# Kernel tuning notes

Measured on AMD Instinct MI355X. Metric: run time of the kernel, lower is better.

Reference implementation:

```python
import jax, jax.numpy as jnp
from jax import lax
import numpy as np

PROPRIO = 48
NPTS = 1024
NP_PROX = 512
NP_DIST = 512
HP = 187  # proximal_feature_dim
HD = 64   # distal_feature_dim
B = 2048
NA = 12
ACTOR_DIMS = [PROPRIO + HP + HD, 1024, 512, 256, 128, NA]


def gru_last(x, wih, whh, bih, bhh):
    """torch-style GRU (gate order r,z,n), returns last hidden. x: [B,T,in]."""
    Bx, T, _ = x.shape
    H = whh.shape[1]
    gx = x @ wih.T + bih  # [B,T,3H], input projections precomputed
    def step(h, gxt):
        gh = h @ whh.T + bhh
        r = jax.nn.sigmoid(gxt[:, :H] + gh[:, :H])
        z = jax.nn.sigmoid(gxt[:, H:2 * H] + gh[:, H:2 * H])
        n = jnp.tanh(gxt[:, 2 * H:] + r * gh[:, 2 * H:])
        return (1.0 - z) * n + z * h, None
    h0 = jnp.zeros((Bx, H), x.dtype)
    hT, _ = lax.scan(step, h0, jnp.swapaxes(gx, 0, 1))
    return hT


def _encode(pts, w1, b1, w2, b2):
    h = jax.nn.elu(pts @ w1.T + b1)
    return jax.nn.elu(h @ w2.T + b2)


def _forward(obs, pe_prox_w1, pe_prox_b1, pe_prox_w2, pe_prox_b2,
             pe_dist_w1, pe_dist_b1, pe_dist_w2, pe_dist_b2,
             gru_prox_wih, gru_prox_whh, gru_prox_bih, gru_prox_bhh,
             gru_dist_wih, gru_dist_whh, gru_dist_bih, gru_dist_bhh,
             mem_prox_wih, mem_prox_whh, mem_prox_bih, mem_prox_bhh,
             mem_dist_wih, mem_dist_whh, mem_dist_bih, mem_dist_bhh,
             actor_w0, actor_b0, actor_w1, actor_b1, actor_w2, actor_b2,
             actor_w3, actor_b3, actor_w4, actor_b4,
             prox_idx, dist_idx):
    proprio = obs[:, :PROPRIO]
    lidar = obs[:, PROPRIO:].reshape(obs.shape[0], NPTS, 3)  # history_length=1
    # irregular gather of proximal/distal point subsets (sampling plan buffers)
    prox_enc = _encode(lidar[:, prox_idx], pe_prox_w1, pe_prox_b1, pe_prox_w2, pe_prox_b2)  # [B,512,64]
    dist_enc = _encode(lidar[:, dist_idx], pe_dist_w1, pe_dist_b1, pe_dist_w2, pe_dist_b2)  # [B,512,64]
    # spatial GRUs over the point sequence
    hp = gru_last(prox_enc, gru_prox_wih, gru_prox_whh, gru_prox_bih, gru_prox_bhh)  # [B,187]
    hd = gru_last(dist_enc, gru_dist_wih, gru_dist_whh, gru_dist_bih, gru_dist_bhh)  # [B,64]
    # temporal memory GRUs (single step, zero initial hidden)
    fp = gru_last(hp[:, None, :], mem_prox_wih, mem_prox_whh, mem_prox_bih, mem_prox_bhh)
    fd = gru_last(hd[:, None, :], mem_dist_wih, mem_dist_whh, mem_dist_bih, mem_dist_bhh)
    x = jnp.concatenate([proprio, fp, fd], axis=-1)  # [B,299]
    for w, b in ((actor_w0, actor_b0), (actor_w1, actor_b1), (actor_w2, actor_b2), (actor_w3, actor_b3)):
        x = jax.nn.elu(x @ w.T + b)
    return x @ actor_w4.T + actor_b4  # action mean [B,12]


def setup_inputs() -> dict:
    key = jax.random.key(0)
    ks = iter(jax.random.split(key, 64))
    def n(shape, scale=0.05):
        return (jax.random.normal(next(ks), shape, jnp.float32) * scale)
    inp = {}
    inp["obs"] = jax.random.normal(next(ks), (B, PROPRIO + NPTS * 3), jnp.float32)
    inp["prox_idx"] = jax.random.randint(next(ks), (NP_PROX,), 0, NPTS)
    inp["dist_idx"] = jax.random.randint(next(ks), (NP_DIST,), 0, NPTS)
    for pfx in ("pe_prox", "pe_dist"):
        inp[pfx + "_w1"] = n((64, 3)); inp[pfx + "_b1"] = jnp.zeros((64,), jnp.float32)
        inp[pfx + "_w2"] = n((64, 64)); inp[pfx + "_b2"] = jnp.zeros((64,), jnp.float32)
    for pfx, H, din in (("gru_prox", HP, 64), ("gru_dist", HD, 64), ("mem_prox", HP, HP), ("mem_dist", HD, HD)):
        inp[pfx + "_wih"] = n((3 * H, din)); inp[pfx + "_whh"] = n((3 * H, H))
        inp[pfx + "_bih"] = jnp.zeros((3 * H,), jnp.float32); inp[pfx + "_bhh"] = jnp.zeros((3 * H,), jnp.float32)
    for i, (di, do) in enumerate(zip(ACTOR_DIMS[:-1], ACTOR_DIMS[1:])):
        inp[f"actor_w{i}"] = n((do, di)); inp[f"actor_b{i}"] = jnp.zeros((do,), jnp.float32)
    return inp


def reference(obs, prox_idx, dist_idx,
              pe_prox_w1, pe_prox_b1, pe_prox_w2, pe_prox_b2,
              pe_dist_w1, pe_dist_b1, pe_dist_w2, pe_dist_b2,
              gru_prox_wih, gru_prox_whh, gru_prox_bih, gru_prox_bhh,
              gru_dist_wih, gru_dist_whh, gru_dist_bih, gru_dist_bhh,
              mem_prox_wih, mem_prox_whh, mem_prox_bih, mem_prox_bhh,
              mem_dist_wih, mem_dist_whh, mem_dist_bih, mem_dist_bhh,
              actor_w0, actor_b0, actor_w1, actor_b1, actor_w2, actor_b2,
              actor_w3, actor_b3, actor_w4, actor_b4):
    return _forward(obs, pe_prox_w1, pe_prox_b1, pe_prox_w2, pe_prox_b2,
                    pe_dist_w1, pe_dist_b1, pe_dist_w2, pe_dist_b2,
                    gru_prox_wih, gru_prox_whh, gru_prox_bih, gru_prox_bhh,
                    gru_dist_wih, gru_dist_whh, gru_dist_bih, gru_dist_bhh,
                    mem_prox_wih, mem_prox_whh, mem_prox_bih, mem_prox_bhh,
                    mem_dist_wih, mem_dist_whh, mem_dist_bih, mem_dist_bhh,
                    actor_w0, actor_b0, actor_w1, actor_b1, actor_w2, actor_b2,
                    actor_w3, actor_b3, actor_w4, actor_b4,
                    prox_idx, dist_idx)
```

## Files before the change

### kernel.cpp

```cpp
#include <hip/hip_runtime.h>
#include <stdint.h>

typedef __attribute__((ext_vector_type(8))) short short8;
typedef __attribute__((ext_vector_type(4))) float f32x4;

#define DEV __device__ __forceinline__

#define L2E 1.4426950408889634f

DEV unsigned short f2bf(float f) {
    union { float f; uint32_t u; } v; v.f = f;
    return (unsigned short)((v.u + 0x7FFFu + ((v.u >> 16) & 1u)) >> 16);
}
DEV float sig_(float x) {
    return __builtin_amdgcn_rcpf(1.f + __builtin_amdgcn_exp2f(-L2E * x));
}
DEV float tanh_(float x) {
    return 1.f - 2.f * __builtin_amdgcn_rcpf(1.f + __builtin_amdgcn_exp2f(2.f * L2E * x));
}
DEV float elu_(float x) {
    return x > 0.f ? x : __builtin_amdgcn_exp2f(L2E * x) - 1.f;
}
DEV f32x4 splat4(float v) { f32x4 r; r[0]=v; r[1]=v; r[2]=v; r[3]=v; return r; }
DEV void pin(short8& v) { asm volatile("" : "+v"(v)); }

struct PJob { const float* s; unsigned short* d; int Hs, NG, Ks, Kd, total; };
struct PJobs { PJob j[11]; };

__global__ __launch_bounds__(256) void pack_all(PJobs P)
{
    PJob jb = P.j[blockIdx.y];
    int e = blockIdx.x * 256 + threadIdx.x;
    if (e >= jb.total) return;
    int n = e / jb.Kd, k = e - n * jb.Kd;
    int g = n / jb.NG, jj = n - g * jb.NG;
    float v = (jj < jb.Hs && k < jb.Ks) ? jb.s[(size_t)(g * jb.Hs + jj) * jb.Ks + k] : 0.f;
    jb.d[e] = f2bf(v);
}

template<int H, int KP>
DEV void gru_body(int blk,
                  const float* __restrict__ obs, const int* __restrict__ idx,
                  const float* __restrict__ w1, const float* __restrict__ b1,
                  const float* __restrict__ w2, const float* __restrict__ b2,
                  const unsigned short* __restrict__ wih, const unsigned short* __restrict__ whh,
                  const float* __restrict__ bih, const float* __restrict__ bhh,
                  unsigned short* __restrict__ houtb, char* smem)
{
    constexpr int NCT = KP / 16;
    constexpr int KS  = KP / 32;
    constexpr int HP8 = KP + 8;

    unsigned short* hlds = (unsigned short*)(smem);
    unsigned short* xs   = (unsigned short*)(smem + 12800);
    unsigned short* h1s  = (unsigned short*)(smem + 17408);
    unsigned short* w2s  = (unsigned short*)(smem + 22016);
    float* ptsb          = (float*)(smem + 31232);
    float* w1s           = (float*)(smem + 31744);
    float* b1s           = (float*)(smem + 32768);
    float* b2s           = (float*)(smem + 33024);

    const int tid  = threadIdx.x;
    const int wave = tid >> 6, lane = tid & 63, quad = lane >> 4, l16 = lane & 15;
    const int b0   = blk * 16;
    const int ct   = wave;
    const bool act = (ct < NCT);
    const int c    = ct * 16 + l16;

    for (int e = tid; e < 2*16*HP8; e += 768) hlds[e] = 0;
    for (int e = tid; e < 4096; e += 768) { int n = e >> 6, k = e & 63; w2s[n*72 + k] = f2bf(w2[e]); }
    if (tid < 192) w1s[(tid/3)*4 + (tid - (tid/3)*3)] = w1[tid];
    if (tid < 64) { b1s[tid] = b1[tid]; b2s[tid] = b2[tid]; }

    const float* myrow = obs + (size_t)(b0 + (tid & 15)) * 3120 + 48;
    float px = 0.f, py = 0.f, pz = 0.f;
    if (tid < 16) {
        int p0 = idx[0];
        ptsb[tid*4 + 0] = myrow[3*p0 + 0];
        ptsb[tid*4 + 1] = myrow[3*p0 + 1];
        ptsb[tid*4 + 2] = myrow[3*p0 + 2];
        int p1 = idx[1];
        px = myrow[3*p1 + 0]; py = myrow[3*p1 + 1]; pz = myrow[3*p1 + 2];
    }

    short8 whr[3][KS];
    short8 wxr[3][2];
    float bsr = 0.f, bsz = 0.f, binx = 0.f, bhnn = 0.f;
    {
        const int cl = act ? c : l16;
#pragma unroll
        for (int g = 0; g < 3; ++g) {
#pragma unroll
            for (int ks = 0; ks < KS; ++ks)
                whr[g][ks] = *(const short8*)(whh + ((size_t)(g*KP + cl))*KP + ks*32 + quad*8);
#pragma unroll
            for (int ks = 0; ks < 2; ++ks)
                wxr[g][ks] = *(const short8*)(wih + ((size_t)(g*KP + cl))*64 + ks*32 + quad*8);
        }
    }
#pragma unroll
    for (int g = 0; g < 3; ++g) {
#pragma unroll
        for (int ks = 0; ks < KS; ++ks) pin(whr[g][ks]);
#pragma unroll
        for (int ks = 0; ks < 2; ++ks)  pin(wxr[g][ks]);
    }
    if (act && c < H) {
        bsr  = bih[c]       + bhh[c];
        bsz  = bih[H + c]   + bhh[H + c];
        binx = bih[2*H + c];
        bhnn = bhh[2*H + c];
    }
    float hreg[4] = {0.f, 0.f, 0.f, 0.f};

    __syncthreads();

    int cur = 0;
    for (int i = 0; i < 514; ++i) {
        if (i < 512) {
            const float* pt = ptsb + (i & 1) * 64;
            unsigned short* h1w = h1s + (i & 1) * (16*72);
#pragma unroll
            for (int e = tid; e < 1024; e += 768) {
                int p = e >> 6, ch = e & 63;
                float v = w1s[ch*4+0]*pt[p*4+0] + w1s[ch*4+1]*pt[p*4+1]
                        + w1s[ch*4+2]*pt[p*4+2] + b1s[ch];
                h1w[p*72 + ch] = f2bf(elu_(v));
            }
            if (tid < 16) {
                float* dst = ptsb + ((i+1) & 1) * 64 + tid*4;
                dst[0] = px; dst[1] = py; dst[2] = pz;
                int tn = (i + 2 < 512) ? i + 2 : 511;
                int pn = idx[tn];
                px = myrow[3*pn + 0]; py = myrow[3*pn + 1]; pz = myrow[3*pn + 2];
            }
        }
        if (i >= 1 && i < 513 && wave < 4) {
            const unsigned short* h1r = h1s + ((i-1) & 1) * (16*72);
            unsigned short*       xw  = xs  + ((i-1) & 1) * (16*72);
            f32x4 a2 = splat4(0.f);
#pragma unroll
            for (int ks = 0; ks < 2; ++ks) {
                short8 af = *(const short8*)(h1r + l16*72 + ks*32 + quad*8);
                short8 bf = *(const short8*)(w2s + (wave*16 + l16)*72 + ks*32 + quad*8);
                a2 = __builtin_amdgcn_mfma_f32_16x16x32_bf16(af, bf, a2, 0, 0, 0);
            }
            int c2 = wave*16 + l16;
            float b2v = b2s[c2];
#pragma unroll
            for (int j = 0; j < 4; ++j)
                xw[(quad*4 + j)*72 + c2] = f2bf(elu_(a2[j] + b2v));
        }
        if (i >= 2) {
            int t = i - 2;
            const unsigned short* xsr = xs + (t & 1) * (16*72);
            const unsigned short* hc  = hlds + cur * (16*HP8);
            unsigned short*       hn  = hlds + (cur ^ 1) * (16*HP8);
            if (act) {
                f32x4 acc[4];
                acc[0] = splat4(bsr);
                acc[1] = splat4(bsz);
                acc[2] = splat4(binx);
                acc[3] = splat4(bhnn);
#pragma unroll
                for (int ks = 0; ks < 2; ++ks) {
                    short8 xf = *(const short8*)(xsr + l16*72 + ks*32 + quad*8);
                    acc[0] = __builtin_amdgcn_mfma_f32_16x16x32_bf16(xf, wxr[0][ks], acc[0], 0, 0, 0);
                    acc[1] = __builtin_amdgcn_mfma_f32_16x16x32_bf16(xf, wxr[1][ks], acc[1], 0, 0, 0);
                    acc[2] = __builtin_amdgcn_mfma_f32_16x16x32_bf16(xf, wxr[2][ks], acc[2], 0, 0, 0);
                }
#pragma unroll
                for (int ks = 0; ks < KS; ++ks) {
                    short8 ah = *(const short8*)(hc + l16*HP8 + ks*32 + quad*8);
                    acc[0] = __builtin_amdgcn_mfma_f32_16x16x32_bf16(ah, whr[0][ks], acc[0], 0, 0, 0);
                    acc[1] = __builtin_amdgcn_mfma_f32_16x16x32_bf16(ah, whr[1][ks], acc[1], 0, 0, 0);
                    acc[3] = __builtin_amdgcn_mfma_f32_16x16x32_bf16(ah, whr[2][ks], acc[3], 0, 0, 0);
                }
#pragma unroll
                for (int j = 0; j < 4; ++j) {
                    int m = quad*4 + j;
                    float r  = sig_(acc[0][j]);
                    float zg = sig_(acc[1][j]);
                    float nn = tanh_(acc[2][j] + r * acc[3][j]);
                    float hv = nn + zg * (hreg[j] - nn);
                    hreg[j] = hv;
                    hn[m*HP8 + c] = f2bf(hv);
                }
            }
            cur ^= 1;
        }
        __syncthreads();
    }

    if (act)
#pragma unroll
        for (int j = 0; j < 4; ++j) {
            int m = quad*4 + j;
            houtb[(size_t)(b0 + m)*KP + c] = (c < H) ? f2bf(hreg[j]) : 0;
        }
}

__global__ __launch_bounds__(768)
__attribute__((amdgpu_waves_per_eu(3, 3)))
void gru_kernel(
    const float* __restrict__ obs,
    const int* __restrict__ prox_idx, const int* __restrict__ dist_idx,
    const float* __restrict__ w1p, const float* __restrict__ b1p,
    const float* __restrict__ w2p, const float* __restrict__ b2p,
    const float* __restrict__ w1d, const float* __restrict__ b1d,
    const float* __restrict__ w2d, const float* __restrict__ b2d,
    const unsigned short* __restrict__ wihp, const unsigned short* __restrict__ whhp,
    const unsigned short* __restrict__ wihd, const unsigned short* __restrict__ whhd,
    const float* __restrict__ bihp, const float* __restrict__ bhhp,
    const float* __restrict__ bihd, const float* __restrict__ bhhd,
    unsigned short* __restrict__ hpb, unsigned short* __restrict__ hdb)
{
    __shared__ __align__(16) char smem[33280];
    if (blockIdx.x < 128)
        gru_body<187, 192>(blockIdx.x, obs, prox_idx, w1p, b1p, w2p, b2p,
                           wihp, whhp, bihp, bhhp, hpb, smem);
    else
        gru_body<64, 64>(blockIdx.x - 128, obs, dist_idx, w1d, b1d, w2d, b2d,
                         wihd, whhd, bihd, bhhd, hdb, smem);
}

__global__ __launch_bounds__(256) void bgemm_kernel(
    const unsigned short* __restrict__ A, const unsigned short* __restrict__ B,
    const float* __restrict__ bias, void* __restrict__ C,
    int Kp, int Np, int Nstore, int mode)
{
    __shared__ __align__(16) unsigned short Asl[64*40];
    __shared__ __align__(16) unsigned short Bsl[64*40];
    const int tid = threadIdx.x;
    const int wave = tid >> 6, lane = tid & 63, quad = lane >> 4, l16 = lane & 15;
    const int n0 = blockIdx.x * 64, m0 = blockIdx.y * 64;
    const int r = tid >> 2, sg = (tid & 3) * 8;

    f32x4 acc[4];
#pragma unroll
    for (int nt = 0; nt < 4; ++nt) acc[nt] = splat4(0.f);

    for (int k0 = 0; k0 < Kp; k0 += 32) {
        short8 av = *(const short8*)(A + (size_t)(m0 + r)*Kp + k0 + sg);
        short8 bv;
        if (n0 + r < Np) bv = *(const short8*)(B + (size_t)(n0 + r)*Kp + k0 + sg);
        else { short8 z; for (int q = 0; q < 8; ++q) z[q] = 0; bv = z; }
        *(short8*)(Asl + r*40 + sg) = av;
        *(short8*)(Bsl + r*40 + sg) = bv;
        __syncthreads();
        short8 af = *(const short8*)(Asl + (wave*16 + l16)*40 + quad*8);
#pragma unroll
        for (int nt = 0; nt < 4; ++nt) {
            short8 bf = *(const short8*)(Bsl + (nt*16 + l16)*40 + quad*8);
            acc[nt] = __builtin_amdgcn_mfma_f32_16x16x32_bf16(af, bf, acc[nt], 0, 0, 0);
        }
        __syncthreads();
    }
#pragma unroll
    for (int nt = 0; nt < 4; ++nt) {
        int n = n0 + nt*16 + l16;
        float bv = (bias && n < Np) ? bias[n] : 0.f;
#pragma unroll
        for (int j = 0; j < 4; ++j) {
            int m = m0 + wave*16 + quad*4 + j;
            float v = acc[nt][j] + bv;
            if (mode == 1) {
                ((unsigned short*)C)[(size_t)m*Np + n] = f2bf(elu_(v));
            } else {
                if (n < Nstore) ((float*)C)[(size_t)m*Nstore + n] = v;
            }
        }
    }
}

__global__ __launch_bounds__(256) void memcat_kernel(
    const float* __restrict__ obs, const float* __restrict__ Gp, const float* __restrict__ Gd,
    const float* __restrict__ mbip, const float* __restrict__ mbhp,
    const float* __restrict__ mbid, const float* __restrict__ mbhd,
    unsigned short* __restrict__ x0b)
{
    int i = blockIdx.x * 256 + threadIdx.x;
    if (i >= 2048 * 320) return;
    int b = i / 320, cc = i - b * 320;
    float v;
    if (cc < 48) {
        v = obs[(size_t)b*3120 + cc];
    } else if (cc < 235) {
        int j = cc - 48;
        float dr = Gp[(size_t)b*576 + j];
        float dz = Gp[(size_t)b*576 + 192 + j];
        float dn = Gp[(size_t)b*576 + 384 + j];
        float r  = sig_(dr + mbip[j] + mbhp[j]);
        float zg = sig_(dz + mbip[187+j] + mbhp[187+j]);
        float nn = tanh_(dn + mbip[374+j] + r * mbhp[374+j]);
        v = (1.f - zg) * nn;
    } else if (cc < 299) {
        int j = cc - 235;
        float dr = Gd[(size_t)b*192 + j];
        float dz = Gd[(size_t)b*192 + 64 + j];
        float dn = Gd[(size_t)b*192 + 128 + j];
        float r  = sig_(dr + mbid[j] + mbhd[j]);
        float zg = sig_(dz + mbid[64+j] + mbhd[64+j]);
        float nn = tanh_(dn + mbid[128+j] + r * mbhd[128+j]);
        v = (1.f - zg) * nn;
    } else {
        v = 0.f;
    }
    x0b[i] = f2bf(v);
}

extern "C" void kernel_launch(void* const* d_in, const int* in_sizes, int n_in,
                              void* d_out, int out_size, void* d_ws, size_t ws_size,
                              hipStream_t stream)
{
    (void)in_sizes; (void)n_in; (void)out_size; (void)ws_size;
    const float* obs        = (const float*)d_in[0];
    const int*   prox_idx   = (const int*)d_in[1];
    const int*   dist_idx   = (const int*)d_in[2];
    const float* pe_prox_w1 = (const float*)d_in[3];
    const float* pe_prox_b1 = (const float*)d_in[4];
    const float* pe_prox_w2 = (const float*)d_in[5];
    const float* pe_prox_b2 = (const float*)d_in[6];
    const float* pe_dist_w1 = (const float*)d_in[7];
    const float* pe_dist_b1 = (const float*)d_in[8];
    const float* pe_dist_w2 = (const float*)d_in[9];
    const float* pe_dist_b2 = (const float*)d_in[10];
    const float* gp_wih = (const float*)d_in[11];
    const float* gp_whh = (const float*)d_in[12];
    const float* gp_bih = (const float*)d_in[13];
    const float* gp_bhh = (const float*)d_in[14];
    const float* gd_wih = (const float*)d_in[15];
    const float* gd_whh = (const float*)d_in[16];
    const float* gd_bih = (const float*)d_in[17];
    const float* gd_bhh = (const float*)d_in[18];
    const float* mp_wih = (const float*)d_in[19];
    const float* mp_bih = (const float*)d_in[21];
    const float* mp_bhh = (const float*)d_in[22];
    const float* md_wih = (const float*)d_in[23];
    const float* md_bih = (const float*)d_in[25];
    const float* md_bhh = (const float*)d_in[26];
    const float* aw0 = (const float*)d_in[27]; const float* ab0 = (const float*)d_in[28];
    const float* aw1 = (const float*)d_in[29]; const float* ab1 = (const float*)d_in[30];
    const float* aw2 = (const float*)d_in[31]; const float* ab2 = (const float*)d_in[32];
    const float* aw3 = (const float*)d_in[33]; const float* ab3 = (const float*)d_in[34];
    const float* aw4 = (const float*)d_in[35]; const float* ab4 = (const float*)d_in[36];
    float* out = (float*)d_out;

    char* ws = (char*)d_ws;
    size_t off = 0;
    auto alloc = [&](size_t bytes) -> char* {
        char* p = ws + off;
        off = (off + bytes + 255) & ~(size_t)255;
        return p;
    };
    unsigned short* wih_p = (unsigned short*)alloc(36864*2);
    unsigned short* whh_p = (unsigned short*)alloc(110592*2);
    unsigned short* wih_d = (unsigned short*)alloc(12288*2);
    unsigned short* whh_d = (unsigned short*)alloc(12288*2);
    unsigned short* mw_p  = (unsigned short*)alloc(110592*2);
    unsigned short* mw_d  = (unsigned short*)alloc(12288*2);
    unsigned short* w0p   = (unsigned short*)alloc((size_t)1024*320*2);
    unsigned short* w1p   = (unsigned short*)alloc((size_t)512*1024*2);
    unsigned short* w2p   = (unsigned short*)alloc((size_t)256*512*2);
    unsigned short* w3p   = (unsigned short*)alloc((size_t)128*256*2);
    unsigned short* w4p   = (unsigned short*)alloc((size_t)16*128*2);
    unsigned short* hpb   = (unsigned short*)alloc((size_t)2048*192*2);
    unsigned short* hdb   = (unsigned short*)alloc((size_t)2048*64*2);
    float* Gp             = (float*)alloc((size_t)2048*576*4);
    float* Gd             = (float*)alloc((size_t)2048*192*4);
    unsigned short* x0b   = (unsigned short*)alloc((size_t)2048*320*2);
    unsigned short* a1b   = (unsigned short*)alloc((size_t)2048*1024*2);
    unsigned short* a2b   = (unsigned short*)alloc((size_t)2048*512*2);
    unsigned short* a3b   = (unsigned short*)alloc((size_t)2048*256*2);
    unsigned short* a4b   = (unsigned short*)alloc((size_t)2048*128*2);

    PJobs P;
    P.j[0]  = { gp_wih, wih_p, 187, 192, 64, 64, 36864 };
    P.j[1]  = { gp_whh, whh_p, 187, 192, 187, 192, 110592 };
    P.j[2]  = { gd_wih, wih_d, 64, 64, 64, 64, 12288 };
    P.j[3]  = { gd_whh, whh_d, 64, 64, 64, 64, 12288 };
    P.j[4]  = { mp_wih, mw_p, 187, 192, 187, 192, 110592 };
    P.j[5]  = { md_wih, mw_d, 64, 64, 64, 64, 12288 };
    P.j[6]  = { aw0, w0p, 1024, 1024, 299, 320, 327680 };
    P.j[7]  = { aw1, w1p, 512, 512, 1024, 1024, 524288 };
    P.j[8]  = { aw2, w2p, 256, 256, 512, 512, 131072 };
    P.j[9]  = { aw3, w3p, 128, 128, 256, 256, 32768 };
    P.j[10] = { aw4, w4p, 12, 16, 128, 128, 2048 };
    pack_all<<<dim3(2048, 11), 256, 0, stream>>>(P);

    gru_kernel<<<256, 768, 0, stream>>>(
        obs, prox_idx, dist_idx,
        pe_prox_w1, pe_prox_b1, pe_prox_w2, pe_prox_b2,
        pe_dist_w1, pe_dist_b1, pe_dist_w2, pe_dist_b2,
        wih_p, whh_p, wih_d, whh_d,
        gp_bih, gp_bhh, gd_bih, gd_bhh, hpb, hdb);

    bgemm_kernel<<<dim3(9, 32), 256, 0, stream>>>(hpb, mw_p, nullptr, Gp, 192, 576, 576, 0);
    bgemm_kernel<<<dim3(3, 32), 256, 0, stream>>>(hdb, mw_d, nullptr, Gd, 64, 192, 192, 0);
    memcat_kernel<<<2560, 256, 0, stream>>>(obs, Gp, Gd, mp_bih, mp_bhh, md_bih, md_bhh, x0b);

    bgemm_kernel<<<dim3(16, 32), 256, 0, stream>>>(x0b, w0p, ab0, a1b, 320, 1024, 1024, 1);
    bgemm_kernel<<<dim3(8,  32), 256, 0, stream>>>(a1b, w1p, ab1, a2b, 1024, 512, 512, 1);
    bgemm_kernel<<<dim3(4,  32), 256, 0, stream>>>(a2b, w2p, ab2, a3b, 512, 256, 256, 1);
    bgemm_kernel<<<dim3(2,  32), 256, 0, stream>>>(a3b, w3p, ab3, a4b, 256, 128, 128, 1);
    bgemm_kernel<<<dim3(1,  32), 256, 0, stream>>>(a4b, w4p, ab4, out, 128, 16, 12, 0);
}
```

Before: 867.8 us.

## Precompute proximal point encodings in FP8 and run GRU input projection with FP8 MFMA

Adds a separate encoder kernel that gathers proximal lidar points, runs the two-layer ELU point MLP, and stores the encodings as FP8 in workspace. The proximal GRU then streams these FP8 encodings, keeps the FP8-packed input weights in registers, and uses FP8 MFMA for the input projection, taking the per-step encoder work off the serial recurrence. It also drops the waves_per_eu attribute. The costs are an extra 64MB write and read of encodings, an extra launch, reduced precision on the GRU inputs and weights, and a fallback to the fused path if the workspace is too small.

```diff
diff --git a/kernel.cpp b/kernel.cpp
--- a/kernel.cpp
+++ b/kernel.cpp
@@ -3,6 +3,7 @@
 
 typedef __attribute__((ext_vector_type(8))) short short8;
 typedef __attribute__((ext_vector_type(4))) float f32x4;
+typedef __attribute__((ext_vector_type(4))) unsigned int u32x4;
 
 #define DEV __device__ __forceinline__
 
@@ -12,6 +13,26 @@
     union { float f; uint32_t u; } v; v.f = f;
     return (unsigned short)((v.u + 0x7FFFu + ((v.u >> 16) & 1u)) >> 16);
 }
+DEV uint8_t f2fp8(float f) {
+    union { float f; uint32_t u; } v; v.f = f;
+    uint32_t s = (v.u >> 24) & 0x80u;
+    uint32_t absu = v.u & 0x7FFFFFFFu;
+    int E = (int)(absu >> 23);
+    if (E >= 135 + 1) return (uint8_t)(s | 0x7E);
+    if (E >= 121) {
+        uint32_t m = absu & 0x7FFFFFu;
+        uint32_t keep = m >> 20;
+        uint32_t rest = m & 0xFFFFFu;
+        uint32_t rnd = (rest > 0x80000u || (rest == 0x80000u && (keep & 1u))) ? 1u : 0u;
+        uint32_t mag = (((uint32_t)(E - 120) << 3) | keep) + rnd;
+        if (mag > 0x7Eu) mag = 0x7Eu;
+        return (uint8_t)(s | mag);
+    }
+    float sc = __builtin_fabsf(f) * 512.f;
+    uint32_t m8 = (uint32_t)(sc + 0.5f);
+    if (m8 > 7u) return (uint8_t)(s | 0x08);
+    return (uint8_t)(s | m8);
+}
 DEV float sig_(float x) {
     return __builtin_amdgcn_rcpf(1.f + __builtin_amdgcn_exp2f(-L2E * x));
 }
@@ -23,9 +44,10 @@
 }
 DEV f32x4 splat4(float v) { f32x4 r; r[0]=v; r[1]=v; r[2]=v; r[3]=v; return r; }
 DEV void pin(short8& v) { asm volatile("" : "+v"(v)); }
+DEV void pinl(long& v)  { asm volatile("" : "+v"(v)); }
 
 struct PJob { const float* s; unsigned short* d; int Hs, NG, Ks, Kd, total; };
-struct PJobs { PJob j[11]; };
+struct PJobs { PJob j[12]; };
 
 __global__ __launch_bounds__(256) void pack_all(PJobs P)
 {
@@ -38,8 +60,172 @@
     jb.d[e] = f2bf(v);
 }
 
+__global__ __launch_bounds__(256) void pack_fp8(const float* __restrict__ src,
+                                                uint8_t* __restrict__ dst)
+{
+    int e = blockIdx.x * 256 + threadIdx.x;
+    if (e >= 576 * 64) return;
+    int n = e >> 6, k = e & 63;
+    int g = n / 192, jj = n - g * 192;
+    float v = (jj < 187) ? src[(size_t)(g * 187 + jj) * 64 + k] : 0.f;
+    dst[e] = f2fp8(v);
+}
+
+__global__ __launch_bounds__(256) void enc_kernel(
+    const float* __restrict__ obs, const int* __restrict__ idx,
+    const float* __restrict__ w1, const float* __restrict__ b1,
+    const unsigned short* __restrict__ w2p, const float* __restrict__ b2,
+    uint8_t* __restrict__ enc8)
+{
+    const int b = blockIdx.x, t0 = blockIdx.y * 64;
+    const int tid = threadIdx.x;
+    __shared__ __align__(16) float pts[64][4];
+    __shared__ float w1s[256];
+    __shared__ float b1s[64], b2s[64];
+    __shared__ __align__(16) unsigned short h1s[64][72];
+
+    if (tid < 192) w1s[(tid/3)*4 + (tid - (tid/3)*3)] = w1[tid];
+    if (tid < 64) { b1s[tid] = b1[tid]; b2s[tid] = b2[tid]; }
+    for (int e = tid; e < 192; e += 256) {
+        int p = e / 3, c2 = e - p * 3;
+        int pi = idx[t0 + p];
+        pts[p][c2] = obs[(size_t)b * 3120 + 48 + (size_t)pi * 3 + c2];
+    }
+    __syncthreads();
+#pragma unroll
+    for (int r = 0; r < 16; ++r) {
+        int e = tid + r * 256;
+        int p = e >> 6, ch = e & 63;
+        float v = w1s[ch*4]*pts[p][0] + w1s[ch*4+1]*pts[p][1]
+                + w1s[ch*4+2]*pts[p][2] + b1s[ch];
+        h1s[p][ch] = f2bf(elu_(v));
+    }
+    __syncthreads();
+    const int wave = tid >> 6, lane = tid & 63, quad = lane >> 4, l16 = lane & 15;
+#pragma unroll
+    for (int ct = 0; ct < 4; ++ct) {
+        f32x4 a2 = splat4(0.f);
+#pragma unroll
+        for (int ks = 0; ks < 2; ++ks) {
+            short8 af = *(const short8*)(&h1s[wave*16 + l16][ks*32 + quad*8]);
+            short8 bf = *(const short8*)(w2p + (ct*16 + l16)*64 + ks*32 + quad*8);
+            a2 = __builtin_amdgcn_mfma_f32_16x16x32_bf16(af, bf, a2, 0, 0, 0);
+        }
+        int c = ct*16 + l16;
+        float b2v = b2s[c];
+#pragma unroll
+        for (int j = 0; j < 4; ++j) {
+            int m = wave*16 + quad*4 + j;
+            enc8[((size_t)b*512 + t0 + m)*64 + c] = f2fp8(elu_(a2[j] + b2v));
+        }
+    }
+}
+
+DEV void gru_body_pre(int blk, const uint8_t* __restrict__ enc8,
+                      const uint8_t* __restrict__ wih8,
+                      const unsigned short* __restrict__ whh,
+                      const float* __restrict__ bih, const float* __restrict__ bhh,
+                      unsigned short* __restrict__ houtb, char* smem)
+{
+    constexpr int H = 187, KP = 192, KS = 6, HP8 = 200;
+    unsigned short* hlds = (unsigned short*)smem;
+    uint8_t* xs = (uint8_t*)(smem + 12800);
+
+    const int tid  = threadIdx.x;
+    const int wave = tid >> 6, lane = tid & 63, quad = lane >> 4, l16 = lane & 15;
+    const int b0   = blk * 16;
+    const int c    = wave * 16 + l16;
+
+    for (int e = tid; e < 2*16*HP8; e += 768) hlds[e] = 0;
+
+    short8 whr[3][KS];
+    long   wx8[3][2];
+#pragma unroll
+    for (int g = 0; g < 3; ++g) {
+#pragma unroll
+        for (int ks = 0; ks < KS; ++ks)
+            whr[g][ks] = *(const short8*)(whh + ((size_t)(g*KP + c))*KP + ks*32 + quad*8);
+#pragma unroll
+        for (int ks = 0; ks < 2; ++ks)
+            wx8[g][ks] = *(const long*)(wih8 + ((size_t)(g*KP + c))*64 + ks*32 + quad*8);
+    }
+#pragma unroll
+    for (int g = 0; g < 3; ++g) {
+#pragma unroll
+        for (int ks = 0; ks < KS; ++ks) pin(whr[g][ks]);
+#pragma unroll
+        for (int ks = 0; ks < 2; ++ks)  pinl(wx8[g][ks]);
+    }
+    float bsr = 0.f, bsz = 0.f, binx = 0.f, bhnn = 0.f;
+    if (c < H) {
+        bsr  = bih[c]       + bhh[c];
+        bsz  = bih[H + c]   + bhh[H + c];
+        binx = bih[2*H + c];
+        bhnn = bhh[2*H + c];
+    }
+    float hreg[4] = {0.f, 0.f, 0.f, 0.f};
+
+    u32x4 xq;
+    const int xrow = lane >> 2, xseg = lane & 3;
+    if (wave == 0) {
+        xq = *(const u32x4*)(enc8 + ((size_t)(b0 + xrow)*512 + 0)*64 + xseg*16);
+        *(u32x4*)(xs + 0*1280 + xrow*80 + xseg*16) = xq;
+        xq = *(const u32x4*)(enc8 + ((size_t)(b0 + xrow)*512 + 1)*64 + xseg*16);
+    }
+    __syncthreads();
+
+    int cur = 0;
+    for (int t = 0; t < 512; ++t) {
+        if (wave == 0) {
+            *(u32x4*)(xs + ((t+1)&1)*1280 + xrow*80 + xseg*16) = xq;
+            int tn = (t + 2 < 512) ? t + 2 : 511;
+            xq = *(const u32x4*)(enc8 + ((size_t)(b0 + xrow)*512 + tn)*64 + xseg*16);
+        }
+        const uint8_t* xsr = xs + (t&1)*1280;
+        const unsigned short* hc = hlds + cur * (16*HP8);
+        unsigned short*       hn = hlds + (cur ^ 1) * (16*HP8);
+
+        f32x4 acc[4];
+        acc[0] = splat4(bsr);
+        acc[1] = splat4(bsz);
+        acc[2] = splat4(binx);
+        acc[3] = splat4(bhnn);
+#pragma unroll
+        for (int ks = 0; ks < 2; ++ks) {
+            long a8 = *(const long*)(xsr + l16*80 + ks*32 + quad*8);
+            acc[0] = __builtin_amdgcn_mfma_f32_16x16x32_fp8_fp8(a8, wx8[0][ks], acc[0], 0, 0, 0);
+            acc[1] = __builtin_amdgcn_mfma_f32_16x16x32_fp8_fp8(a8, wx8[1][ks], acc[1], 0, 0, 0);
+            acc[2] = __builtin_amdgcn_mfma_f32_16x16x32_fp8_fp8(a8, wx8[2][ks], acc[2], 0, 0, 0);
+        }
+#pragma unroll
+        for (int ks = 0; ks < KS; ++ks) {
+            short8 ah = *(const short8*)(hc + l16*HP8 + ks*32 + quad*8);
+            acc[0] = __builtin_amdgcn_mfma_f32_16x16x32_bf16(ah, whr[0][ks], acc[0], 0, 0, 0);
+            acc[1] = __builtin_amdgcn_mfma_f32_16x16x32_bf16(ah, whr[1][ks], acc[1], 0, 0, 0);
+            acc[3] = __builtin_amdgcn_mfma_f32_16x16x32_bf16(ah, whr[2][ks], acc[3], 0, 0, 0);
+        }
+#pragma unroll
+        for (int j = 0; j < 4; ++j) {
+            int m = quad*4 + j;
+            float r  = sig_(acc[0][j]);
+            float zg = sig_(acc[1][j]);
+            float nn = tanh_(acc[2][j] + r * acc[3][j]);
+            float hv = nn + zg * (hreg[j] - nn);
+            hreg[j] = hv;
+            hn[m*HP8 + c] = f2bf(hv);
+        }
+        cur ^= 1;
+        __syncthreads();
+    }
+#pragma unroll
+    for (int j = 0; j < 4; ++j) {
+        int m = quad*4 + j;
+        houtb[(size_t)(b0 + m)*KP + c] = (c < H) ? f2bf(hreg[j]) : 0;
+    }
+}
+
 template<int H, int KP>
-DEV void gru_body(int blk,
+DEV void gru_body_fused(int blk,
                   const float* __restrict__ obs, const int* __restrict__ idx,
                   const float* __restrict__ w1, const float* __restrict__ b1,
                   const float* __restrict__ w2, const float* __restrict__ b2,
@@ -200,11 +386,11 @@
         }
 }
 
-__global__ __launch_bounds__(768)
-__attribute__((amdgpu_waves_per_eu(3, 3)))
-void gru_kernel(
+__global__ __launch_bounds__(768) void gru_kernel(
+    int mode,
     const float* __restrict__ obs,
     const int* __restrict__ prox_idx, const int* __restrict__ dist_idx,
+    const uint8_t* __restrict__ encp8, const uint8_t* __restrict__ wihp8,
     const float* __restrict__ w1p, const float* __restrict__ b1p,
     const float* __restrict__ w2p, const float* __restrict__ b2p,
     const float* __restrict__ w1d, const float* __restrict__ b1d,
@@ -216,12 +402,16 @@
     unsigned short* __restrict__ hpb, unsigned short* __restrict__ hdb)
 {
     __shared__ __align__(16) char smem[33280];
-    if (blockIdx.x < 128)
-        gru_body<187, 192>(blockIdx.x, obs, prox_idx, w1p, b1p, w2p, b2p,
-                           wihp, whhp, bihp, bhhp, hpb, smem);
-    else
-        gru_body<64, 64>(blockIdx.x - 128, obs, dist_idx, w1d, b1d, w2d, b2d,
-                         wihd, whhd, bihd, bhhd, hdb, smem);
+    if (blockIdx.x < 128) {
+        if (mode == 0)
+            gru_body_pre(blockIdx.x, encp8, wihp8, whhp, bihp, bhhp, hpb, smem);
+        else
+            gru_body_fused<187, 192>(blockIdx.x, obs, prox_idx, w1p, b1p, w2p, b2p,
+                                     wihp, whhp, bihp, bhhp, hpb, smem);
+    } else {
+        gru_body_fused<64, 64>(blockIdx.x - 128, obs, dist_idx, w1d, b1d, w2d, b2d,
+                               wihd, whhd, bihd, bhhd, hdb, smem);
+    }
 }
 
 __global__ __launch_bounds__(256) void bgemm_kernel(
@@ -313,7 +503,7 @@
                               void* d_out, int out_size, void* d_ws, size_t ws_size,
                               hipStream_t stream)
 {
-    (void)in_sizes; (void)n_in; (void)out_size; (void)ws_size;
+    (void)in_sizes; (void)n_in; (void)out_size;
     const float* obs        = (const float*)d_in[0];
     const int*   prox_idx   = (const int*)d_in[1];
     const int*   dist_idx   = (const int*)d_in[2];
@@ -364,6 +554,8 @@
     unsigned short* w2p   = (unsigned short*)alloc((size_t)256*512*2);
     unsigned short* w3p   = (unsigned short*)alloc((size_t)128*256*2);
     unsigned short* w4p   = (unsigned short*)alloc((size_t)16*128*2);
+    unsigned short* w2e   = (unsigned short*)alloc(4096*2);
+    uint8_t* wih8         = (uint8_t*)alloc(576*64);
     unsigned short* hpb   = (unsigned short*)alloc((size_t)2048*192*2);
     unsigned short* hdb   = (unsigned short*)alloc((size_t)2048*64*2);
     float* Gp             = (float*)alloc((size_t)2048*576*4);
@@ -373,6 +565,8 @@
     unsigned short* a2b   = (unsigned short*)alloc((size_t)2048*512*2);
     unsigned short* a3b   = (unsigned short*)alloc((size_t)2048*256*2);
     unsigned short* a4b   = (unsigned short*)alloc((size_t)2048*128*2);
+    uint8_t* enc8         = (uint8_t*)alloc((size_t)2048*512*64);
+    const int mode = (off <= ws_size) ? 0 : 1;
 
     PJobs P;
     P.j[0]  = { gp_wih, wih_p, 187, 192, 64, 64, 36864 };
@@ -386,10 +580,17 @@
     P.j[8]  = { aw2, w2p, 256, 256, 512, 512, 131072 };
     P.j[9]  = { aw3, w3p, 128, 128, 256, 256, 32768 };
     P.j[10] = { aw4, w4p, 12, 16, 128, 128, 2048 };
-    pack_all<<<dim3(2048, 11), 256, 0, stream>>>(P);
+    P.j[11] = { pe_prox_w2, w2e, 64, 64, 64, 64, 4096 };
+    pack_all<<<dim3(2048, 12), 256, 0, stream>>>(P);
+
+    if (mode == 0) {
+        pack_fp8<<<144, 256, 0, stream>>>(gp_wih, wih8);
+        enc_kernel<<<dim3(2048, 8), 256, 0, stream>>>(
+            obs, prox_idx, pe_prox_w1, pe_prox_b1, w2e, pe_prox_b2, enc8);
+    }
 
     gru_kernel<<<256, 768, 0, stream>>>(
-        obs, prox_idx, dist_idx,
+        mode, obs, prox_idx, dist_idx, enc8, wih8,
         pe_prox_w1, pe_prox_b1, pe_prox_w2, pe_prox_b2,
         pe_dist_w1, pe_dist_b1, pe_dist_w2, pe_dist_b2,
         wih_p, whh_p, wih_d, whh_d,
```

Result: no change. 851.0 us (-1.9%).
